# Kernel tuning notes

Hardware: AMD Instinct MI355X
Metric: run time of the kernel (lower is better)

The kernel has to match this reference:

```python
import jax, jax.numpy as jnp
import numpy as np

I, H, NH, A = 128, 2048, 2, 4   # input_size, hidden_size, n_hidden, alpha_dim
K = 2 * A * A                   # per-position theta entries
B = 8192


def make_masks():
    # MADE sequential-ordering masks, identical to DART.create_masks
    inp = np.arange(I)
    degrees = [inp] + [np.arange(H) % (I - 1) for _ in range(NH + 1)] + [np.arange(I) - 1]
    masks = [(d1[:, None] >= d0[None, :]).astype(np.float32)
             for d0, d1 in zip(degrees[:-1], degrees[1:])]
    # last mask repeated per theta entry: repeat(1, K).view(-1, H) == row-repeat
    masks[-1] = np.repeat(masks[-1], K, axis=0)
    return [jnp.asarray(m) for m in masks]


def setup_inputs() -> dict:
    key = jax.random.key(0)
    ks = jax.random.split(key, 5)
    x = jax.random.normal(ks[0], (B, I), dtype=jnp.float32)

    def lin(k, out_dim, in_dim):
        kw, kb = jax.random.split(k)
        s = 1.0 / np.sqrt(in_dim)
        W = jax.random.uniform(kw, (out_dim, in_dim), minval=-s, maxval=s, dtype=jnp.float32)
        b = jax.random.uniform(kb, (out_dim,), minval=-s, maxval=s, dtype=jnp.float32)
        return W, b

    W0, b0 = lin(ks[1], H, I)
    W1, b1 = lin(ks[2], H, H)
    W2, b2 = lin(ks[3], H, H)
    W3, b3 = lin(ks[4], I * K, H)
    return dict(x=x, W0=W0, b0=b0, W1=W1, b1=b1, W2=W2, b2=b2, W3=W3, b3=b3)


def logexpmm(a, b):
    # log-domain matmul: out[..., i, j] = logsumexp_k(a[..., i, k] + b[..., k, j])
    return jax.nn.logsumexp(a[..., :, :, None] + b[..., None, :, :], axis=-2)


def reference(x, W0, b0, W1, b1, W2, b2, W3, b3):
    m = make_masks()
    h = jax.nn.relu(x @ (m[0] * W0).T + b0)
    h = jax.nn.relu(h @ (m[1] * W1).T + b1)
    h = jax.nn.relu(h @ (m[2] * W2).T + b2)
    theta = (h @ (m[3] * W3).T + b3).reshape(-1, I, 2, A, A)
    mu, alpha = theta[:, :, 0], theta[:, :, 1]  # (B, I, A, A)

    LOG2PI = float(np.log(2.0 * np.pi))
    xe = x[:, :, None, None]
    # Normal(mu, exp(alpha)).log_prob(x) - log(alpha_dim)
    logp = (-0.5 * ((xe - mu) * jnp.exp(-alpha)) ** 2
            - alpha - 0.5 * LOG2PI - jnp.log(jnp.float32(A)))

    first = logp[:, 0, 0:1]        # (B, 1, A)
    last = logp[:, -1, :, 0:1]     # (B, A, 1)
    inner = jnp.swapaxes(logp[:, 1:-1], 0, 1)  # (I-2, B, A, A)

    def step(carry, mtx):
        return logexpmm(carry, mtx), None

    prod, _ = jax.lax.scan(step, inner[0], inner[1:])
    return logexpmm(first, logexpmm(prod, last))  # (B, 1, 1)
```

## Files before the change

### kernel.cpp

```cpp
#include <hip/hip_runtime.h>
#include <hip/hip_bf16.h>
#include <cstdint>
#include <cstddef>

#define AS1 __attribute__((address_space(1)))
#define AS3 __attribute__((address_space(3)))

typedef __bf16 bf16x8 __attribute__((ext_vector_type(8)));
typedef float  floatx4 __attribute__((ext_vector_type(4)));

__device__ __forceinline__ void load_lds16(const void* g, void* l) {
    __builtin_amdgcn_global_load_lds((AS1 void*)g, (AS3 void*)l, 16, 0, 0);
}

__device__ __forceinline__ float fexp2(float x) { return __builtin_amdgcn_exp2f(x); }
__device__ __forceinline__ float flog2(float x) { return __builtin_amdgcn_logf(x); }

__device__ __forceinline__ int invp(int p) {
    return p < 2032 ? (p & 15) * 127 + (p >> 4) : p;
}
__device__ __forceinline__ int resp(int p) {
    return p < 2032 ? (p >> 4) : p - 2032;
}

__global__ __launch_bounds__(256)
void prep_all(const float* __restrict__ x,  const float* __restrict__ W0,
              const float* __restrict__ W1, const float* __restrict__ W2,
              const float* __restrict__ W3,
              __bf16* __restrict__ xb,  __bf16* __restrict__ w0m,
              __bf16* __restrict__ w1m, __bf16* __restrict__ w2m,
              __bf16* __restrict__ w3m)
{
    const int blk = blockIdx.x;
    const float* src; __bf16* dst; int shift, mode; long base;
    if (blk < 4096)        { src = x;  dst = xb;  shift = 7;  mode = 3; base = 0; }
    else if (blk < 5120)   { src = W0; dst = w0m; shift = 7;  mode = 0; base = 4096L * 256; }
    else if (blk < 21504)  { src = W1; dst = w1m; shift = 11; mode = 1; base = 5120L * 256; }
    else if (blk < 37888)  { src = W2; dst = w2m; shift = 11; mode = 1; base = 21504L * 256; }
    else                   { src = W3; dst = w3m; shift = 11; mode = 2; base = 37888L * 256; }
    long idx = (long)blk * 256 + threadIdx.x - base;
    int row = (int)(idx >> shift);
    int col = (int)(idx & ((1 << shift) - 1));
    float v; bool keep;
    if (mode == 3)      { v = src[idx];                                  keep = true; }
    else if (mode == 0) { v = src[(long)invp(row) * 128 + col];          keep = resp(row) >= col; }
    else if (mode == 1) { v = src[(long)invp(row) * 2048 + invp(col)];   keep = resp(row) >= resp(col); }
    else                { v = src[(long)row * 2048 + invp(col)];         keep = (row >> 5) > resp(col); }
    dst[idx] = (__bf16)(keep ? v : 0.0f);
}

template <bool RELU, bool OBF16, bool TLAYOUT, bool PERMBIAS>
__global__ __launch_bounds__(256, 2)
void gemm_bt(const __bf16* __restrict__ A, const __bf16* __restrict__ Bw,
             const float* __restrict__ bias, void* __restrict__ Cout,
             int N, int K, int klm, int kla, int kls, int tail)
{
    __shared__ __align__(16) __bf16 lsA[128 * 32];
    __shared__ __align__(16) __bf16 lsB[128 * 32];
    const int tid  = threadIdx.x;
    const int wave = tid >> 6;
    const int lane = tid & 63;
    const int bm = blockIdx.x, bn = blockIdx.y;
    const int wm = wave >> 1, wn = wave & 1;

    const int rsub = lane >> 2;
    const int cbx  = (lane & 3) ^ ((lane >> 3) & 3);
    const __bf16* gsrc[4];
    __bf16* ldst[4];
#pragma unroll
    for (int t = 0; t < 4; ++t) {
        int j = wave * 4 + t;
        if (j < 8) {
            int row = bm * 128 + j * 16 + rsub;
            gsrc[t] = A + (size_t)row * K + cbx * 8;
            ldst[t] = lsA + j * 512;
        } else {
            int jj = j - 8;
            int row = bn * 128 + jj * 16 + rsub;
            gsrc[t] = Bw + (size_t)row * K + cbx * 8;
            ldst[t] = lsB + jj * 512;
        }
    }

    const int fr   = lane & 15;
    const int ks   = lane >> 4;
    const int slot = ks ^ ((fr >> 1) & 3);
    const __bf16* ardp[4];
    const __bf16* brdp[4];
#pragma unroll
    for (int i = 0; i < 4; ++i) {
        ardp[i] = lsA + (wm * 64 + i * 16 + fr) * 32 + slot * 8;
        brdp[i] = lsB + (wn * 64 + i * 16 + fr) * 32 + slot * 8;
    }

    floatx4 acc[4][4];
    const floatx4 vzero = {0.f, 0.f, 0.f, 0.f};
#pragma unroll
    for (int mi = 0; mi < 4; ++mi)
#pragma unroll
        for (int ni = 0; ni < 4; ++ni) acc[mi][ni] = vzero;

    const int nk = K >> 5;
    int limit = (klm * bn + kla) >> kls;
    if (limit > nk) limit = nk;
    const int iters = limit + ((tail && limit < nk) ? 1 : 0);

    for (int it = 0; it < iters; ++it) {
        const int kt = (it < limit ? it : nk - 1) << 5;
        __syncthreads();
#pragma unroll
        for (int t = 0; t < 4; ++t)
            load_lds16((const void*)(gsrc[t] + kt), (void*)ldst[t]);
        __syncthreads();
        bf16x8 af[4], bf[4];
#pragma unroll
        for (int i = 0; i < 4; ++i) af[i] = *(const bf16x8*)ardp[i];
#pragma unroll
        for (int i = 0; i < 4; ++i) bf[i] = *(const bf16x8*)brdp[i];
#pragma unroll
        for (int mi = 0; mi < 4; ++mi)
#pragma unroll
            for (int ni = 0; ni < 4; ++ni)
                acc[mi][ni] = __builtin_amdgcn_mfma_f32_16x16x32_bf16(
                    af[mi], bf[ni], acc[mi][ni], 0, 0, 0);
    }

    const int cn  = lane & 15;
    const int cr4 = (lane >> 4) * 4;
#pragma unroll
    for (int ni = 0; ni < 4; ++ni) {
        int col = bn * 128 + wn * 64 + ni * 16 + cn;
        float bv = bias[PERMBIAS ? invp(col) : col];
#pragma unroll
        for (int mi = 0; mi < 4; ++mi) {
            int row0 = bm * 128 + wm * 64 + mi * 16 + cr4;
#pragma unroll
            for (int q = 0; q < 4; ++q) {
                float v = acc[mi][ni][q] + bv;
                if (RELU) v = fmaxf(v, 0.f);
                if (TLAYOUT) {
                    size_t addr = (size_t)(bm * 2 + wm) * ((size_t)N * 64)
                                + (size_t)col * 64 + (mi * 16 + cr4 + q);
                    ((float*)Cout)[addr] = v;
                } else if (OBF16) {
                    ((__bf16*)Cout)[(size_t)(row0 + q) * N + col] = (__bf16)v;
                } else {
                    ((float*)Cout)[(size_t)(row0 + q) * N + col] = v;
                }
            }
        }
    }
}

__global__ __launch_bounds__(256)
void chain_seg(const float* __restrict__ th2,
               const float* __restrict__ x,
               float* __restrict__ P)
{
    const int b = blockIdx.x * 256 + threadIdx.x;
    const int s = blockIdx.y;
    const int i0 = 1 + s * 7;
    const float* tp = th2 + (size_t)(b >> 6) * (4096 * 64) + (b & 63)
                          + (size_t)i0 * 32 * 64;
    const float* xp = x + (size_t)b * 128 + i0;

    const float LOG2E = 1.4426950408889634f;
    const float C0    = 2.3052328943245633f;

    float M[4][4];
#pragma unroll
    for (int r = 0; r < 4; ++r)
#pragma unroll
        for (int c = 0; c < 4; ++c) M[r][c] = (r == c) ? 0.f : -1e30f;

    for (int ii = 0; ii < 7; ++ii) {
        float mu[16], al[16];
#pragma unroll
        for (int j = 0; j < 16; ++j) mu[j] = tp[(size_t)j * 64];
#pragma unroll
        for (int j = 0; j < 16; ++j) al[j] = tp[(size_t)(16 + j) * 64];
        float xv = xp[ii];
        tp += 32 * 64;
        float lp[16];
#pragma unroll
        for (int j = 0; j < 16; ++j) {
            float a = al[j];
            float e = fexp2(-a * LOG2E);
            float z = (xv - mu[j]) * e;
            lp[j] = (-0.5f * z * z - a - C0) * LOG2E;
        }
        float Mn[4][4];
#pragma unroll
        for (int r = 0; r < 4; ++r)
#pragma unroll
            for (int c = 0; c < 4; ++c) {
                float a0 = M[r][0] + lp[0 * 4 + c];
                float a1 = M[r][1] + lp[1 * 4 + c];
                float a2 = M[r][2] + lp[2 * 4 + c];
                float a3 = M[r][3] + lp[3 * 4 + c];
                float mx = fmaxf(fmaxf(a0, a1), fmaxf(a2, a3));
                float sm = fexp2(a0 - mx) + fexp2(a1 - mx) +
                           fexp2(a2 - mx) + fexp2(a3 - mx);
                Mn[r][c] = mx + flog2(sm);
            }
#pragma unroll
        for (int r = 0; r < 4; ++r)
#pragma unroll
            for (int c = 0; c < 4; ++c) M[r][c] = Mn[r][c];
    }

    float* pb = P + ((size_t)b * 18 + s) * 16;
#pragma unroll
    for (int r = 0; r < 4; ++r) {
        floatx4 o = {M[r][0], M[r][1], M[r][2], M[r][3]};
        *(floatx4*)(pb + r * 4) = o;
    }
}

__global__ __launch_bounds__(256)
void chain_fin(const float* __restrict__ th2,
               const float* __restrict__ x,
               const float* __restrict__ P,
               float* __restrict__ out)
{
    const int tid  = threadIdx.x;
    const int lane = tid & 63;
    const int r    = lane & 3;
    const int l0   = lane & 60;
    const int b    = blockIdx.x * 64 + (tid >> 2);
    const float* tb = th2 + (size_t)(b >> 6) * (4096 * 64) + (b & 63);

    const float LOG2E = 1.4426950408889634f;
    const float LN2   = 0.6931471805599453f;
    const float C0    = 2.3052328943245633f;

    const float* Pb = P + (size_t)b * 288;
    floatx4 m0 = *(const floatx4*)(Pb + r * 4);
    float M[4] = {m0[0], m0[1], m0[2], m0[3]};

#pragma unroll
    for (int s = 1; s < 18; ++s) {
        floatx4 lr = *(const floatx4*)(Pb + s * 16 + r * 4);
        float Mn[4];
#pragma unroll
        for (int c = 0; c < 4; ++c) {
            float a0 = M[0] + __shfl(lr[c], l0 + 0);
            float a1 = M[1] + __shfl(lr[c], l0 + 1);
            float a2 = M[2] + __shfl(lr[c], l0 + 2);
            float a3 = M[3] + __shfl(lr[c], l0 + 3);
            float mx = fmaxf(fmaxf(a0, a1), fmaxf(a2, a3));
            float sm = fexp2(a0 - mx) + fexp2(a1 - mx) + fexp2(a2 - mx) + fexp2(a3 - mx);
            Mn[c] = mx + flog2(sm);
        }
#pragma unroll
        for (int k = 0; k < 4; ++k) M[k] = Mn[k];
    }

    float xl = x[(size_t)b * 128 + 127];
    float a[4];
#pragma unroll
    for (int c = 0; c < 4; ++c) {
        float mu_ = tb[(size_t)(4064 + c * 4) * 64];
        float al_ = tb[(size_t)(4064 + 16 + c * 4) * 64];
        float e = fexp2(-al_ * LOG2E);
        float z = (xl - mu_) * e;
        float lp2 = (-0.5f * z * z - al_ - C0) * LOG2E;
        a[c] = M[c] + lp2;
    }
    float mx = fmaxf(fmaxf(a[0], a[1]), fmaxf(a[2], a[3]));
    float tr = mx + flog2(fexp2(a[0] - mx) + fexp2(a[1] - mx) +
                          fexp2(a[2] - mx) + fexp2(a[3] - mx));

    float x0  = x[(size_t)b * 128];
    float muf = tb[(size_t)r * 64];
    float alf = tb[(size_t)(16 + r) * 64];
    float ef = fexp2(-alf * LOG2E);
    float zf = (x0 - muf) * ef;
    float f2 = (-0.5f * zf * zf - alf - C0) * LOG2E;
    float v = f2 + tr;
    float m1 = fmaxf(v, __shfl_xor(v, 1));
    float m2 = fmaxf(m1, __shfl_xor(m1, 2));
    float sum = fexp2(v - m2);
    sum += __shfl_xor(sum, 1);
    sum += __shfl_xor(sum, 2);
    if (r == 0) out[b] = (m2 + flog2(sum)) * LN2;
}

extern "C" void kernel_launch(void* const* d_in, const int* in_sizes, int n_in,
                              void* d_out, int out_size, void* d_ws, size_t ws_size,
                              hipStream_t stream)
{
    (void)in_sizes; (void)n_in; (void)out_size; (void)ws_size;
    const float* x  = (const float*)d_in[0];
    const float* W0 = (const float*)d_in[1];
    const float* b0 = (const float*)d_in[2];
    const float* W1 = (const float*)d_in[3];
    const float* b1 = (const float*)d_in[4];
    const float* W2 = (const float*)d_in[5];
    const float* b2 = (const float*)d_in[6];
    const float* W3 = (const float*)d_in[7];
    const float* b3 = (const float*)d_in[8];

    char* ws = (char*)d_ws;
    size_t off = 0;
    auto alloc = [&](size_t bytes) { char* p = ws + off; off += bytes; return p; };
    __bf16* xb  = (__bf16*)alloc((size_t)8192 * 128 * 2);
    __bf16* w0m = (__bf16*)alloc((size_t)2048 * 128 * 2);
    __bf16* w1m = (__bf16*)alloc((size_t)2048 * 2048 * 2);
    __bf16* w2m = (__bf16*)alloc((size_t)2048 * 2048 * 2);
    __bf16* w3m = (__bf16*)alloc((size_t)4096 * 2048 * 2);
    __bf16* h1  = (__bf16*)alloc((size_t)8192 * 2048 * 2);
    __bf16* h2  = (__bf16*)alloc((size_t)8192 * 2048 * 2);
    float*  th  = (float*) alloc((size_t)8192 * 4096 * 4);
    __bf16* h3  = h1;
    float*  P   = (float*)h2;

    prep_all<<<70656, 256, 0, stream>>>(x, W0, W1, W2, W3, xb, w0m, w1m, w2m, w3m);

    gemm_bt<true, true, false, true><<<dim3(64, 16), 256, 0, stream>>>(
        xb, w0m, b0, h1, 2048, 128, 8, 39, 5, 0);
    gemm_bt<true, true, false, true><<<dim3(64, 16), 256, 0, stream>>>(
        h1, w1m, b1, h2, 2048, 2048, 4, 4, 0, 1);
    gemm_bt<true, true, false, true><<<dim3(64, 16), 256, 0, stream>>>(
        h2, w2m, b2, h3, 2048, 2048, 4, 4, 0, 1);
    gemm_bt<false, false, true, false><<<dim3(64, 32), 256, 0, stream>>>(
        h3, w3m, b3, th, 4096, 2048, 2, 2, 0, 1);

    chain_seg<<<dim3(32, 18), 256, 0, stream>>>(th, x, P);
    chain_fin<<<128, 256, 0, stream>>>(th, x, P, (float*)d_out);
}
```

Measured before the change: 389.1 us.

## Vectorize weight prep via LDS row gather, store theta in bf16, raise occupancy

The prep kernel now handles one row per block and uses 8-wide vector loads and stores. For the permuted weight matrices it stages the source row in LDS and gathers from there, replacing the per-element scattered global reads. The theta output of the last GEMM is stored as bf16 instead of fp32, which halves its write traffic and the reads in the chain kernels. The GEMM launch bounds go from 2 to 4 waves per SIMD. Storing theta in bf16 loses precision in mu and alpha before the exponentials, which could affect accuracy, and the higher occupancy target may force register spills.

After: 357.6 us. 1.09x faster.

```diff
diff --git a/kernel.cpp b/kernel.cpp
--- a/kernel.cpp
+++ b/kernel.cpp
@@ -31,26 +31,71 @@
               __bf16* __restrict__ w1m, __bf16* __restrict__ w2m,
               __bf16* __restrict__ w3m)
 {
+    __shared__ float lds[2048];
     const int blk = blockIdx.x;
-    const float* src; __bf16* dst; int shift, mode; long base;
-    if (blk < 4096)        { src = x;  dst = xb;  shift = 7;  mode = 3; base = 0; }
-    else if (blk < 5120)   { src = W0; dst = w0m; shift = 7;  mode = 0; base = 4096L * 256; }
-    else if (blk < 21504)  { src = W1; dst = w1m; shift = 11; mode = 1; base = 5120L * 256; }
-    else if (blk < 37888)  { src = W2; dst = w2m; shift = 11; mode = 1; base = 21504L * 256; }
-    else                   { src = W3; dst = w3m; shift = 11; mode = 2; base = 37888L * 256; }
-    long idx = (long)blk * 256 + threadIdx.x - base;
-    int row = (int)(idx >> shift);
-    int col = (int)(idx & ((1 << shift) - 1));
-    float v; bool keep;
-    if (mode == 3)      { v = src[idx];                                  keep = true; }
-    else if (mode == 0) { v = src[(long)invp(row) * 128 + col];          keep = resp(row) >= col; }
-    else if (mode == 1) { v = src[(long)invp(row) * 2048 + invp(col)];   keep = resp(row) >= resp(col); }
-    else                { v = src[(long)row * 2048 + invp(col)];         keep = (row >> 5) > resp(col); }
-    dst[idx] = (__bf16)(keep ? v : 0.0f);
+    const int tid = threadIdx.x;
+    const int t8  = tid * 8;
+
+    if (blk < 640) {
+        bf16x8 o;
+        if (blk < 512) {
+            size_t base = (size_t)blk * 2048 + t8;
+            floatx4 a = *(const floatx4*)(x + base);
+            floatx4 b = *(const floatx4*)(x + base + 4);
+#pragma unroll
+            for (int j = 0; j < 4; ++j) { o[j] = (__bf16)a[j]; o[4 + j] = (__bf16)b[j]; }
+            *(bf16x8*)(xb + base) = o;
+        } else {
+            long idx = (long)(blk - 512) * 2048 + t8;
+            int p_n = (int)(idx >> 7);
+            int c   = (int)(idx & 127);
+            int dg  = resp(p_n);
+            const float* s = W0 + (long)invp(p_n) * 128 + c;
+            floatx4 a = *(const floatx4*)s;
+            floatx4 b = *(const floatx4*)(s + 4);
+#pragma unroll
+            for (int j = 0; j < 8; ++j) {
+                float v = j < 4 ? a[j] : b[j - 4];
+                o[j] = (__bf16)((dg >= c + j) ? v : 0.0f);
+            }
+            *(bf16x8*)(w0m + idx) = o;
+        }
+        return;
+    }
+
+    const float* srow; __bf16* drow; int deg_n; bool strict;
+    if (blk < 2688) {
+        int p_n = blk - 640;
+        srow = W1 + (size_t)invp(p_n) * 2048; drow = w1m + (size_t)p_n * 2048;
+        deg_n = resp(p_n); strict = false;
+    } else if (blk < 4736) {
+        int p_n = blk - 2688;
+        srow = W2 + (size_t)invp(p_n) * 2048; drow = w2m + (size_t)p_n * 2048;
+        deg_n = resp(p_n); strict = false;
+    } else {
+        int n = blk - 4736;
+        srow = W3 + (size_t)n * 2048; drow = w3m + (size_t)n * 2048;
+        deg_n = n >> 5; strict = true;
+    }
+    floatx4 a = *(const floatx4*)(srow + t8);
+    floatx4 b = *(const floatx4*)(srow + t8 + 4);
+    *(floatx4*)&lds[t8]     = a;
+    *(floatx4*)&lds[t8 + 4] = b;
+    __syncthreads();
+    bf16x8 o;
+#pragma unroll
+    for (int j = 0; j < 8; ++j) {
+        int p = t8 + j;
+        float v = lds[invp(p)];
+        int dg = resp(p);
+        bool keep = strict ? (deg_n > dg) : (deg_n >= dg);
+        o[j] = (__bf16)(keep ? v : 0.0f);
+    }
+    *(bf16x8*)(drow + t8) = o;
 }
 
 template <bool RELU, bool OBF16, bool TLAYOUT, bool PERMBIAS>
-__global__ __launch_bounds__(256, 2)
+__global__ __launch_bounds__(256, 4)
 void gemm_bt(const __bf16* __restrict__ A, const __bf16* __restrict__ Bw,
              const float* __restrict__ bias, void* __restrict__ Cout,
              int N, int K, int klm, int kla, int kls, int tail)
@@ -141,7 +186,7 @@
                 if (TLAYOUT) {
                     size_t addr = (size_t)(bm * 2 + wm) * ((size_t)N * 64)
                                 + (size_t)col * 64 + (mi * 16 + cr4 + q);
-                    ((float*)Cout)[addr] = v;
+                    ((__bf16*)Cout)[addr] = (__bf16)v;
                 } else if (OBF16) {
                     ((__bf16*)Cout)[(size_t)(row0 + q) * N + col] = (__bf16)v;
                 } else {
@@ -153,15 +198,15 @@
 }
 
 __global__ __launch_bounds__(256)
-void chain_seg(const float* __restrict__ th2,
+void chain_seg(const __bf16* __restrict__ th2,
                const float* __restrict__ x,
                float* __restrict__ P)
 {
     const int b = blockIdx.x * 256 + threadIdx.x;
     const int s = blockIdx.y;
     const int i0 = 1 + s * 7;
-    const float* tp = th2 + (size_t)(b >> 6) * (4096 * 64) + (b & 63)
-                          + (size_t)i0 * 32 * 64;
+    const __bf16* tp = th2 + (size_t)(b >> 6) * (4096 * 64) + (b & 63)
+                           + (size_t)i0 * 32 * 64;
     const float* xp = x + (size_t)b * 128 + i0;
 
     const float LOG2E = 1.4426950408889634f;
@@ -176,9 +221,9 @@
     for (int ii = 0; ii < 7; ++ii) {
         float mu[16], al[16];
 #pragma unroll
-        for (int j = 0; j < 16; ++j) mu[j] = tp[(size_t)j * 64];
-#pragma unroll
-        for (int j = 0; j < 16; ++j) al[j] = tp[(size_t)(16 + j) * 64];
+        for (int j = 0; j < 16; ++j) mu[j] = (float)tp[(size_t)j * 64];
+#pragma unroll
+        for (int j = 0; j < 16; ++j) al[j] = (float)tp[(size_t)(16 + j) * 64];
         float xv = xp[ii];
         tp += 32 * 64;
         float lp[16];
@@ -218,7 +263,7 @@
 }
 
 __global__ __launch_bounds__(256)
-void chain_fin(const float* __restrict__ th2,
+void chain_fin(const __bf16* __restrict__ th2,
                const float* __restrict__ x,
                const float* __restrict__ P,
                float* __restrict__ out)
@@ -228,7 +273,7 @@
     const int r    = lane & 3;
     const int l0   = lane & 60;
     const int b    = blockIdx.x * 64 + (tid >> 2);
-    const float* tb = th2 + (size_t)(b >> 6) * (4096 * 64) + (b & 63);
+    const __bf16* tb = th2 + (size_t)(b >> 6) * (4096 * 64) + (b & 63);
 
     const float LOG2E = 1.4426950408889634f;
     const float LN2   = 0.6931471805599453f;
@@ -260,8 +305,8 @@
     float a[4];
 #pragma unroll
     for (int c = 0; c < 4; ++c) {
-        float mu_ = tb[(size_t)(4064 + c * 4) * 64];
-        float al_ = tb[(size_t)(4064 + 16 + c * 4) * 64];
+        float mu_ = (float)tb[(size_t)(4064 + c * 4) * 64];
+        float al_ = (float)tb[(size_t)(4064 + 16 + c * 4) * 64];
         float e = fexp2(-al_ * LOG2E);
         float z = (xl - mu_) * e;
         float lp2 = (-0.5f * z * z - al_ - C0) * LOG2E;
@@ -272,8 +317,8 @@
                           fexp2(a[2] - mx) + fexp2(a[3] - mx));
 
     float x0  = x[(size_t)b * 128];
-    float muf = tb[(size_t)r * 64];
-    float alf = tb[(size_t)(16 + r) * 64];
+    float muf = (float)tb[(size_t)r * 64];
+    float alf = (float)tb[(size_t)(16 + r) * 64];
     float ef = fexp2(-alf * LOG2E);
     float zf = (x0 - muf) * ef;
     float f2 = (-0.5f * zf * zf - alf - C0) * LOG2E;
@@ -311,11 +356,11 @@
     __bf16* w3m = (__bf16*)alloc((size_t)4096 * 2048 * 2);
     __bf16* h1  = (__bf16*)alloc((size_t)8192 * 2048 * 2);
     __bf16* h2  = (__bf16*)alloc((size_t)8192 * 2048 * 2);
-    float*  th  = (float*) alloc((size_t)8192 * 4096 * 4);
+    __bf16* th  = (__bf16*)alloc((size_t)8192 * 4096 * 2);
     __bf16* h3  = h1;
     float*  P   = (float*)h2;
 
-    prep_all<<<70656, 256, 0, stream>>>(x, W0, W1, W2, W3, xb, w0m, w1m, w2m, w3m);
+    prep_all<<<8832, 256, 0, stream>>>(x, W0, W1, W2, W3, xb, w0m, w1m, w2m, w3m);
 
     gemm_bt<true, true, false, true><<<dim3(64, 16), 256, 0, stream>>>(
         xb, w0m, b0, h1, 2048, 128, 8, 39, 5, 0);
```
